# Performance work log

Hardware: AMD Instinct MI355X
Metric: run time of the kernel (lower is better)

## Reference

```python
import jax, jax.numpy as jnp
import numpy as np

N_ATOMS = 200000
N_EDGES = 6400000
N_TYPES = 4
COULOMB = 14.399645478425668  # e^2 / (4 pi eps0) in eV*Angstrom
P_EXP = 0.23
A0 = 0.4685


def _phi(r, c, da):
    # r: (E,), c: (4,), da: (4, E) -> (E,)
    return jnp.sum(c[:, None] * jnp.exp(-r * da), axis=0)


def _dphi(r, c, da):
    return jnp.sum(-c[:, None] * da * jnp.exp(-r * da), axis=0)


def _d2phi(r, c, da):
    return jnp.sum(c[:, None] * da ** 2 * jnp.exp(-r * da), axis=0)


def setup_inputs() -> dict:
    key = jax.random.key(0)
    k1, k2, k3, k4 = jax.random.split(key, 4)
    rij = jax.random.uniform(k1, (N_EDGES,), dtype=jnp.float32) * 2.0 + 0.1
    first_atom = jax.random.randint(k2, (N_EDGES,), 0, N_ATOMS, dtype=jnp.int32)
    second_atom = jax.random.randint(k3, (N_EDGES,), 0, N_ATOMS, dtype=jnp.int32)
    atom_type_index = jax.random.randint(k4, (N_ATOMS,), 0, N_TYPES, dtype=jnp.int32)
    # ASE covalent radii for H, C, N, O (Angstrom) and atomic numbers
    covalent_radii = jnp.array([0.31, 0.76, 0.71, 0.66], dtype=jnp.float32)
    atomic_numbers = jnp.array([1.0, 6.0, 7.0, 8.0], dtype=jnp.float32)
    return {
        "rij": rij,
        "covalent_radii": covalent_radii,
        "atomic_numbers": atomic_numbers,
        "first_atom": first_atom,
        "second_atom": second_atom,
        "atom_type_index": atom_type_index,
        "n_atoms": N_ATOMS,
    }


def reference(rij, covalent_radii, atomic_numbers, first_atom, second_atom, atom_type_index, n_atoms):
    # ZBL 4-term exponential screening coefficients
    c = jnp.array([0.02817, 0.28022, 0.50986, 0.18175], dtype=rij.dtype)
    d = jnp.array([0.20162, 0.4029, 0.94229, 3.1998], dtype=rij.dtype)

    ti = atom_type_index[first_atom]   # (E,)
    tj = atom_type_index[second_atom]  # (E,)
    zi = atomic_numbers[ti]
    zj = atomic_numbers[tj]
    rc = covalent_radii[ti] + covalent_radii[tj]  # outer cutoff per pair

    a = A0 / (zi ** P_EXP + zj ** P_EXP)  # (E,)
    da = d[:, None] / a                    # (4, E)
    factor = COULOMB * zi * zj             # (E,)

    # energy at rij
    e = factor / rij * _phi(rij, c, da)

    # switching polynomial matched at rc (r1 = 0)
    phi_c = _phi(rc, c, da)
    dphi_c = _dphi(rc, c, da)
    d2phi_c = _d2phi(rc, c, da)
    ec = factor / rc * phi_c
    dec = factor / rc * (-phi_c / rc + dphi_c)
    d2ec = factor / rc * (d2phi_c - 2.0 / rc * dphi_c + 2.0 * phi_c / rc ** 2)

    A = (-3.0 * dec + rc * d2ec) / rc ** 2
    B = (2.0 * dec - rc * d2ec) / rc ** 3
    C = -ec + rc * dec / 2.0 - rc * rc * d2ec / 12.0

    e = e + A / 3.0 * rij ** 3 + B / 4.0 * rij ** 4 + C
    e = e / 2.0
    e = jnp.where(rij > rc, jnp.zeros_like(e), e)

    # scatter pair energies onto first atom of each pair
    e_nodes = jax.ops.segment_sum(e, first_atom, num_segments=n_atoms)
    return e_nodes
```

## Files before the change

### kernel.cpp

```cpp
#include <hip/hip_runtime.h>

#define TPB_PACK  256
#define P1_BLOCKS 512
#define P1_TPB    1024
#define SB_BITS   14
#define SBS       (1 << SB_BITS)
#define NS_MAX    16
#define P2_TPB    1024
#define R_SUB     39
#define TPB_RED   256
#define CAP_MAX   1024

#define TAB_N   258
#define TAB_L0  (-3.3219281f)
#define TAB_HL  (0.017157490f)
#define TAB_INV (58.283567f)
#define TAB_OFF (193.61423f)

__global__ __launch_bounds__(TPB_PACK) void zbl_pack(
    const int* __restrict__ types, unsigned int* __restrict__ packed,
    float* __restrict__ fallback, int natoms, int nwords)
{
    int tid = blockIdx.x * TPB_PACK + threadIdx.x;
    int nth = gridDim.x * TPB_PACK;
    for (int w = tid; w < nwords; w += nth) {
        int base = w << 4;
        unsigned int word = 0;
        #pragma unroll
        for (int j = 0; j < 16; ++j) {
            int i = base + j;
            unsigned int t = (i < natoms) ? (unsigned int)types[i] : 0u;
            word |= (t & 3u) << (2 * j);
        }
        packed[w] = word;
    }
    for (int i = tid; i < natoms; i += nth) fallback[i] = 0.0f;
}

__global__ __launch_bounds__(P1_TPB) void zbl_bin(
    const float* __restrict__ rij,
    const float* __restrict__ rcov,
    const float* __restrict__ znum,
    const int*  __restrict__ fa,
    const int*  __restrict__ sa,
    const unsigned int* __restrict__ packed,
    unsigned int* __restrict__ regions,
    int*   __restrict__ counts,
    float* __restrict__ fallback,
    int E, int nquad, int natoms, int nwords, int NS, int cap, int chunkQ)
{
    extern __shared__ unsigned int s_packed[];
    __shared__ float  tabE[16 * TAB_N];
    __shared__ float4 cB[16];
    __shared__ float4 cS[16];
    __shared__ float  cC[16];
    __shared__ int scnt[NS_MAX];

    for (int w = threadIdx.x; w < nwords; w += P1_TPB)
        s_packed[w] = packed[w];
    if (threadIdx.x < NS) scnt[threadIdx.x] = 0;

    if (threadIdx.x < 16) {
        const float cc[4] = {0.02817f, 0.28022f, 0.50986f, 0.18175f};
        const float dd[4] = {0.20162f, 0.4029f, 0.94229f, 3.1998f};
        const float COUL = 14.399645478425668f;
        int t = threadIdx.x;
        int ti = t >> 2, tj = t & 3;
        float zi = znum[ti], zj = znum[tj];
        float rc = rcov[ti] + rcov[tj];
        float a = 0.4685f / (powf(zi, 0.23f) + powf(zj, 0.23f));
        float inva = 1.0f / a;
        float factor = COUL * zi * zj;
        float da[4], ee[4];
        float phi = 0.0f, dphi = 0.0f, d2phi = 0.0f;
        #pragma unroll
        for (int k = 0; k < 4; ++k) {
            da[k] = dd[k] * inva;
            ee[k] = expf(-rc * da[k]);
            phi   += cc[k] * ee[k];
            dphi  -= cc[k] * da[k] * ee[k];
            d2phi += cc[k] * da[k] * da[k] * ee[k];
        }
        float invrc = 1.0f / rc;
        float ec   = factor * invrc * phi;
        float dec  = factor * invrc * (-phi * invrc + dphi);
        float d2ec = factor * invrc * (d2phi - 2.0f * invrc * dphi + 2.0f * phi * invrc * invrc);
        float A = (-3.0f * dec + rc * d2ec) * invrc * invrc;
        float B = (2.0f * dec - rc * d2ec) * invrc * invrc * invrc;
        float Cc = -ec + 0.5f * rc * dec - rc * rc * d2ec * (1.0f / 12.0f);
        const float L2E = 1.4426950408889634f;
        cB[t] = make_float4(rc, 0.5f * factor, A * (1.0f / 6.0f), B * 0.125f);
        cS[t] = make_float4(-da[0] * L2E, -da[1] * L2E, -da[2] * L2E, -da[3] * L2E);
        cC[t] = Cc * 0.5f;
    }
    __syncthreads();

    const float lc0 = -5.1497481f;
    const float lc1 = -1.8353434f;
    const float lc2 = -0.9718340f;
    const float lc3 = -2.4600449f;

    for (int n = threadIdx.x; n < 16 * TAB_N; n += P1_TPB) {
        int t = n / TAB_N, k = n - t * TAB_N;
        float v = 0.0f;
        if (k <= 256) {
            float r = exp2f(__builtin_fmaf((float)k, TAB_HL, TAB_L0));
            float4 B = cB[t];
            if (r <= B.x) {
                float4 S = cS[t];
                float p = exp2f(__builtin_fmaf(r, S.x, lc0))
                        + exp2f(__builtin_fmaf(r, S.y, lc1))
                        + exp2f(__builtin_fmaf(r, S.z, lc2))
                        + exp2f(__builtin_fmaf(r, S.w, lc3));
                float r3 = r * r * r;
                float poly = __builtin_fmaf(__builtin_fmaf(B.w, r, B.z), r3, cC[t]);
                v = __builtin_fmaf(B.y * p, 1.0f / r, poly);
            }
        }
        tabE[n] = v;
    }
    __syncthreads();

    const float4* rij4 = (const float4*)rij;
    const int4*   fa4  = (const int4*)fa;
    const int4*   sa4  = (const int4*)sa;

    size_t myreg = (size_t)blockIdx.x * NS;

    int q0 = blockIdx.x * chunkQ;
    int q1 = q0 + chunkQ; if (q1 > nquad) q1 = nquad;

    for (int q = q0 + threadIdx.x; q < q1; q += P1_TPB) {
        float4 rv = rij4[q];
        int4   iv = fa4[q];
        int4   jv = sa4[q];
        float ra[4] = {rv.x, rv.y, rv.z, rv.w};
        int   ia[4] = {iv.x, iv.y, iv.z, iv.w};
        int   ja[4] = {jv.x, jv.y, jv.z, jv.w};
        float eo[4];
        #pragma unroll
        for (int k = 0; k < 4; ++k) {
            int i = ia[k], j = ja[k];
            unsigned int wi = s_packed[i >> 4], wj = s_packed[j >> 4];
            unsigned int ti = (wi >> ((i & 15) * 2)) & 3u;
            unsigned int tj = (wj >> ((j & 15) * 2)) & 3u;
            int t = (int)((ti << 2) | tj);
            float kf = __builtin_fmaf(__log2f(ra[k]), TAB_INV, TAB_OFF);
            int ki = (int)kf;
            ki = ki < 0 ? 0 : (ki > 256 ? 256 : ki);
            float frac = kf - (float)ki;
            int base = t * TAB_N + ki;
            float v0 = tabE[base];
            float v1 = tabE[base + 1];
            eo[k] = __builtin_fmaf(v1 - v0, frac, v0);
        }
        #pragma unroll
        for (int k = 0; k < 4; ++k) {
            if (eo[k] != 0.0f) {
                int atom = ia[k];
                int s = atom >> SB_BITS;
                int slot = atomicAdd(&scnt[s], 1);
                if (slot < cap) {
                    unsigned rec = ((__float_as_uint(eo[k]) + 0x2000u) & 0xFFFFC000u)
                                 | (unsigned)(atom & (SBS - 1));
                    regions[(myreg + s) * (size_t)cap + slot] = rec;
                } else {
                    unsafeAtomicAdd(&fallback[atom], eo[k]);
                }
            }
        }
    }

    if (blockIdx.x == 0) {
        for (int idx = nquad * 4 + threadIdx.x; idx < E; idx += P1_TPB) {
            int i = fa[idx], j = sa[idx];
            unsigned int wi = s_packed[i >> 4], wj = s_packed[j >> 4];
            int t = (int)((((wi >> ((i & 15) * 2)) & 3u) << 2) |
                           ((wj >> ((j & 15) * 2)) & 3u));
            float r = rij[idx];
            float kf = __builtin_fmaf(__log2f(r), TAB_INV, TAB_OFF);
            int ki = (int)kf;
            ki = ki < 0 ? 0 : (ki > 256 ? 256 : ki);
            float frac = kf - (float)ki;
            int base = t * TAB_N + ki;
            float v0 = tabE[base], v1 = tabE[base + 1];
            float e = __builtin_fmaf(v1 - v0, frac, v0);
            if (e != 0.0f) unsafeAtomicAdd(&fallback[i], e);
        }
    }

    __syncthreads();
    if (cap > 0 && threadIdx.x < NS)
        counts[threadIdx.x * P1_BLOCKS + blockIdx.x] = min(scnt[threadIdx.x], cap);
}

__global__ __launch_bounds__(P2_TPB) void zbl_agg(
    const unsigned int* __restrict__ regions,
    const int*  __restrict__ counts,
    float* __restrict__ partials,
    int NS, int cap)
{
    __shared__ float acc[SBS];
    int s = blockIdx.x;
    int r = blockIdx.y;

    float4* acc4 = (float4*)acc;
    for (int i = threadIdx.x; i < SBS / 4; i += P2_TPB)
        acc4[i] = make_float4(0.f, 0.f, 0.f, 0.f);
    __syncthreads();

    int wave = threadIdx.x >> 6;
    int lane = threadIdx.x & 63;
    const int NW = P2_TPB >> 6;
    for (int p = r + wave * R_SUB; p < P1_BLOCKS; p += NW * R_SUB) {
        int n = counts[s * P1_BLOCKS + p];
        size_t base = ((size_t)p * NS + s) * (size_t)cap;
        for (int t = lane; t < n; t += 64) {
            unsigned rec = regions[base + t];
            atomicAdd(&acc[rec & (SBS - 1)],
                      __uint_as_float(rec & 0xFFFFC000u));
        }
    }
    __syncthreads();

    float4* dst4 = (float4*)(partials + ((size_t)s * R_SUB + r) * SBS);
    for (int i = threadIdx.x; i < SBS / 4; i += P2_TPB)
        dst4[i] = acc4[i];
}

__global__ __launch_bounds__(TPB_RED) void zbl_red(
    const float* __restrict__ partials,
    const float* __restrict__ fallback,
    float* __restrict__ out,
    int natoms)
{
    int q = blockIdx.x * TPB_RED + threadIdx.x;
    int nq = natoms >> 2;
    if (q < nq) {
        int atom = q << 2;
        int s = atom >> SB_BITS, i = atom & (SBS - 1);
        const float4* fb4 = (const float4*)(fallback + atom);
        float4 acc = *fb4;
        const float* p = partials + (size_t)s * R_SUB * SBS + i;
        #pragma unroll
        for (int k = 0; k < R_SUB; ++k) {
            float4 v = *(const float4*)(p + (size_t)k * SBS);
            acc.x += v.x; acc.y += v.y; acc.z += v.z; acc.w += v.w;
        }
        *(float4*)(out + atom) = acc;
    }
    if (blockIdx.x == 0 && threadIdx.x < (natoms & 3)) {
        int atom = (nq << 2) + threadIdx.x;
        int s = atom >> SB_BITS, i = atom & (SBS - 1);
        float acc = fallback[atom];
        const float* p = partials + (size_t)s * R_SUB * SBS + i;
        #pragma unroll
        for (int k = 0; k < R_SUB; ++k) acc += p[(size_t)k * SBS];
        out[atom] = acc;
    }
}

extern "C" void kernel_launch(void* const* d_in, const int* in_sizes, int n_in,
                              void* d_out, int out_size, void* d_ws, size_t ws_size,
                              hipStream_t stream) {
    const float* rij  = (const float*)d_in[0];
    const float* rcov = (const float*)d_in[1];
    const float* znum = (const float*)d_in[2];
    const int*   fa   = (const int*)d_in[3];
    const int*   sa   = (const int*)d_in[4];
    const int*   types= (const int*)d_in[5];
    float* out = (float*)d_out;
    int E = in_sizes[0];
    int natoms = out_size;
    int nquad = E / 4;
    int nwords = (natoms + 15) / 16;
    int NS = (natoms + SBS - 1) >> SB_BITS;
    if (NS > NS_MAX) NS = NS_MAX;
    int chunkQ = (nquad + P1_BLOCKS - 1) / P1_BLOCKS;

    size_t packed_bytes = ((size_t)nwords * 4 + 255) & ~(size_t)255;
    size_t cnt_bytes    = ((size_t)NS * P1_BLOCKS * 4 + 255) & ~(size_t)255;
    size_t fb_bytes     = ((size_t)natoms * 4 + 255) & ~(size_t)255;
    size_t part_bytes   = ((size_t)NS * R_SUB * SBS * 4 + 255) & ~(size_t)255;
    unsigned int* packed = (unsigned int*)d_ws;
    int*   counts   = (int*)  ((char*)d_ws + packed_bytes);
    float* fallback = (float*)((char*)d_ws + packed_bytes + cnt_bytes);
    float* partials = (float*)((char*)d_ws + packed_bytes + cnt_bytes + fb_bytes);
    unsigned int* regions = (unsigned int*)((char*)d_ws + packed_bytes + cnt_bytes
                                            + fb_bytes + part_bytes);

    long long avail = (long long)ws_size
                    - (long long)(packed_bytes + cnt_bytes + fb_bytes + part_bytes);
    int cap = 0;
    if (avail > 0) cap = (int)(avail / ((long long)P1_BLOCKS * (long long)NS * 4));
    if (cap > CAP_MAX) cap = CAP_MAX;

    size_t smem = (size_t)nwords * sizeof(unsigned int);

    if (cap >= 64) {
        zbl_pack<<<96, TPB_PACK, 0, stream>>>(types, packed, fallback, natoms, nwords);
        zbl_bin<<<P1_BLOCKS, P1_TPB, smem, stream>>>(
            rij, rcov, znum, fa, sa, packed, regions, counts, fallback,
            E, nquad, natoms, nwords, NS, cap, chunkQ);
        dim3 g2(NS, R_SUB);
        zbl_agg<<<g2, P2_TPB, 0, stream>>>(regions, counts, partials, NS, cap);
        int nq = natoms >> 2;
        zbl_red<<<(nq + TPB_RED - 1) / TPB_RED, TPB_RED, 0, stream>>>(
            partials, fallback, out, natoms);
    } else {
        zbl_pack<<<96, TPB_PACK, 0, stream>>>(types, packed, out, natoms, nwords);
        zbl_bin<<<P1_BLOCKS, P1_TPB, smem, stream>>>(
            rij, rcov, znum, fa, sa, packed, regions, counts, out,
            E, nquad, natoms, nwords, NS, 0, chunkQ);
    }
}
```

Baseline: 162.5 us.

## Fuse pack, bin, aggregate and reduce into one persistent kernel with flag handoffs

Replaces the four-kernel pipeline with a single 512-block kernel. Blocks hand off data through self-validating 64-bit flag words (value plus its complement) in global memory and spin-wait on them, instead of relying on kernel boundaries. Overflow records now go to per-block lists that the final reduction applies, replacing global atomics into a fallback buffer. This is meant to remove launch gaps and tail idle time between stages. It depends on all 512 blocks being co-resident, otherwise the spin-waits can deadlock. It also relies on the workspace flags not already looking valid from a previous call.

```diff
diff --git a/kernel.cpp b/kernel.cpp
--- a/kernel.cpp
+++ b/kernel.cpp
@@ -1,10 +1,12 @@
 #include <hip/hip_runtime.h>
+
 
 #define TPB_PACK  256
 #define P1_BLOCKS 512
 #define P1_TPB    1024
 #define SB_BITS   14
 #define SBS       (1 << SB_BITS)
+#define NS_MEGA   13
 #define NS_MAX    16
 #define P2_TPB    1024
 #define R_SUB     39
@@ -16,6 +18,308 @@
 #define TAB_HL  (0.017157490f)
 #define TAB_INV (58.283567f)
 #define TAB_OFF (193.61423f)
+
+typedef unsigned long long u64;
+
+__device__ __forceinline__ void pub_pair(u64* p, unsigned v) {
+    u64 w = (u64)v | ((u64)(~v) << 32);
+    __hip_atomic_store(p, w, __ATOMIC_RELAXED, __HIP_MEMORY_SCOPE_AGENT);
+}
+__device__ __forceinline__ unsigned spin_pair(u64* p) {
+    for (;;) {
+        u64 w = __hip_atomic_load(p, __ATOMIC_RELAXED, __HIP_MEMORY_SCOPE_AGENT);
+        if ((unsigned)(w >> 32) == ~(unsigned)w) return (unsigned)w;
+        __builtin_amdgcn_s_sleep(1);
+    }
+}
+
+__global__ __launch_bounds__(P1_TPB, 8) void zbl_mega(
+    const float* __restrict__ rij,
+    const float* __restrict__ rcov,
+    const float* __restrict__ znum,
+    const int*  __restrict__ fa,
+    const int*  __restrict__ sa,
+    const int*  __restrict__ types,
+    u64*  __restrict__ packed2,
+    u64*  __restrict__ counts2,
+    u64*  __restrict__ ovfc2,
+    u64*  __restrict__ done2,
+    unsigned int* __restrict__ regions,
+    uint2* __restrict__ ovf,
+    float* __restrict__ partials,
+    float* __restrict__ out,
+    int E, int nquad, int natoms, int nwords, int NS, int cap, int chunkQ,
+    int ovfStride)
+{
+    __shared__ union {
+        struct { unsigned pk[NS_MEGA * SBS / 16]; float tabE[16 * TAB_N]; } a;
+        float  acc[SBS];
+        float4 acc4[SBS / 4];
+    } u;
+    __shared__ float4 cB[16];
+    __shared__ float4 cS[16];
+    __shared__ float  cC[16];
+    __shared__ int    scnt[NS_MAX];
+    __shared__ int    s_ovfn;
+    __shared__ int    s_anyovf;
+
+    const int b   = blockIdx.x;
+    const int tid = threadIdx.x;
+
+    {
+        int wpb = (nwords + P1_BLOCKS - 1) / P1_BLOCKS;
+        int w0 = b * wpb, w1 = w0 + wpb; if (w1 > nwords) w1 = nwords;
+        for (int w = w0 + tid; w < w1; w += P1_TPB) {
+            int base = w << 4;
+            unsigned word = 0;
+            #pragma unroll
+            for (int j = 0; j < 16; ++j) {
+                int i = base + j;
+                unsigned t = (i < natoms) ? (unsigned)types[i] : 0u;
+                word |= (t & 3u) << (2 * j);
+            }
+            pub_pair(&packed2[w], word);
+        }
+    }
+
+    if (tid < NS)  scnt[tid] = 0;
+    if (tid == 32) s_ovfn = 0;
+
+    if (tid < 16) {
+        const float cc[4] = {0.02817f, 0.28022f, 0.50986f, 0.18175f};
+        const float dd[4] = {0.20162f, 0.4029f, 0.94229f, 3.1998f};
+        const float COUL = 14.399645478425668f;
+        int t = tid;
+        int ti = t >> 2, tj = t & 3;
+        float zi = znum[ti], zj = znum[tj];
+        float rc = rcov[ti] + rcov[tj];
+        float a = 0.4685f / (powf(zi, 0.23f) + powf(zj, 0.23f));
+        float inva = 1.0f / a;
+        float factor = COUL * zi * zj;
+        float da[4], ee[4];
+        float phi = 0.0f, dphi = 0.0f, d2phi = 0.0f;
+        #pragma unroll
+        for (int k = 0; k < 4; ++k) {
+            da[k] = dd[k] * inva;
+            ee[k] = expf(-rc * da[k]);
+            phi   += cc[k] * ee[k];
+            dphi  -= cc[k] * da[k] * ee[k];
+            d2phi += cc[k] * da[k] * da[k] * ee[k];
+        }
+        float invrc = 1.0f / rc;
+        float ec   = factor * invrc * phi;
+        float dec  = factor * invrc * (-phi * invrc + dphi);
+        float d2ec = factor * invrc * (d2phi - 2.0f * invrc * dphi + 2.0f * phi * invrc * invrc);
+        float A = (-3.0f * dec + rc * d2ec) * invrc * invrc;
+        float B = (2.0f * dec - rc * d2ec) * invrc * invrc * invrc;
+        float Cc = -ec + 0.5f * rc * dec - rc * rc * d2ec * (1.0f / 12.0f);
+        const float L2E = 1.4426950408889634f;
+        cB[t] = make_float4(rc, 0.5f * factor, A * (1.0f / 6.0f), B * 0.125f);
+        cS[t] = make_float4(-da[0] * L2E, -da[1] * L2E, -da[2] * L2E, -da[3] * L2E);
+        cC[t] = Cc * 0.5f;
+    }
+
+    for (int w = tid; w < nwords; w += P1_TPB)
+        u.a.pk[w] = spin_pair(&packed2[w]);
+    __syncthreads();
+
+    const float lc0 = -5.1497481f;
+    const float lc1 = -1.8353434f;
+    const float lc2 = -0.9718340f;
+    const float lc3 = -2.4600449f;
+
+    for (int n = tid; n < 16 * TAB_N; n += P1_TPB) {
+        int t = n / TAB_N, k = n - t * TAB_N;
+        float v = 0.0f;
+        if (k <= 256) {
+            float r = exp2f(__builtin_fmaf((float)k, TAB_HL, TAB_L0));
+            float4 B = cB[t];
+            if (r <= B.x) {
+                float4 S = cS[t];
+                float p = exp2f(__builtin_fmaf(r, S.x, lc0))
+                        + exp2f(__builtin_fmaf(r, S.y, lc1))
+                        + exp2f(__builtin_fmaf(r, S.z, lc2))
+                        + exp2f(__builtin_fmaf(r, S.w, lc3));
+                float r3 = r * r * r;
+                float poly = __builtin_fmaf(__builtin_fmaf(B.w, r, B.z), r3, cC[t]);
+                v = __builtin_fmaf(B.y * p, 1.0f / r, poly);
+            }
+        }
+        u.a.tabE[n] = v;
+    }
+    __syncthreads();
+
+    {
+        const float4* rij4 = (const float4*)rij;
+        const int4*   fa4  = (const int4*)fa;
+        const int4*   sa4  = (const int4*)sa;
+        int myreg = b * NS;
+        int q0 = b * chunkQ;
+        int q1 = q0 + chunkQ; if (q1 > nquad) q1 = nquad;
+
+        for (int q = q0 + tid; q < q1; q += P1_TPB) {
+            float4 rv = rij4[q];
+            int4   iv = fa4[q];
+            int4   jv = sa4[q];
+            float ra[4] = {rv.x, rv.y, rv.z, rv.w};
+            int   ia[4] = {iv.x, iv.y, iv.z, iv.w};
+            int   ja[4] = {jv.x, jv.y, jv.z, jv.w};
+            float eo[4];
+            #pragma unroll
+            for (int k = 0; k < 4; ++k) {
+                int i = ia[k], j = ja[k];
+                unsigned wi = u.a.pk[i >> 4], wj = u.a.pk[j >> 4];
+                unsigned ti = (wi >> ((i & 15) * 2)) & 3u;
+                unsigned tj = (wj >> ((j & 15) * 2)) & 3u;
+                int t = (int)((ti << 2) | tj);
+                float kf = __builtin_fmaf(__log2f(ra[k]), TAB_INV, TAB_OFF);
+                int ki = (int)kf;
+                ki = ki < 0 ? 0 : (ki > 256 ? 256 : ki);
+                float frac = kf - (float)ki;
+                int base = t * TAB_N + ki;
+                float v0 = u.a.tabE[base];
+                float v1 = u.a.tabE[base + 1];
+                eo[k] = __builtin_fmaf(v1 - v0, frac, v0);
+            }
+            #pragma unroll
+            for (int k = 0; k < 4; ++k) {
+                if (eo[k] != 0.0f) {
+                    int atom = ia[k];
+                    int s = atom >> SB_BITS;
+                    int slot = atomicAdd(&scnt[s], 1);
+                    if (slot < cap) {
+                        unsigned rec = ((__float_as_uint(eo[k]) + 0x2000u) & 0xFFFFC000u)
+                                     | (unsigned)(atom & (SBS - 1));
+                        regions[(myreg + s) * cap + slot] = rec;
+                    } else {
+                        int o = atomicAdd(&s_ovfn, 1);
+                        ovf[(size_t)b * ovfStride + o] =
+                            make_uint2(__float_as_uint(eo[k]), (unsigned)atom);
+                    }
+                }
+            }
+        }
+
+        if (b == 0) {
+            for (int idx = nquad * 4 + tid; idx < E; idx += P1_TPB) {
+                int i = fa[idx], j = sa[idx];
+                unsigned wi = u.a.pk[i >> 4], wj = u.a.pk[j >> 4];
+                int t = (int)((((wi >> ((i & 15) * 2)) & 3u) << 2) |
+                               ((wj >> ((j & 15) * 2)) & 3u));
+                float r = rij[idx];
+                float kf = __builtin_fmaf(__log2f(r), TAB_INV, TAB_OFF);
+                int ki = (int)kf;
+                ki = ki < 0 ? 0 : (ki > 256 ? 256 : ki);
+                float frac = kf - (float)ki;
+                int base = t * TAB_N + ki;
+                float e = __builtin_fmaf(u.a.tabE[base + 1] - u.a.tabE[base], frac,
+                                         u.a.tabE[base]);
+                if (e != 0.0f) {
+                    int o = atomicAdd(&s_ovfn, 1);
+                    ovf[(size_t)b * ovfStride + o] =
+                        make_uint2(__float_as_uint(e), (unsigned)i);
+                }
+            }
+        }
+
+        __syncthreads();
+        if (tid == 0) __threadfence();
+        __syncthreads();
+        if (tid < NS)  pub_pair(&counts2[tid * P1_BLOCKS + b],
+                                (unsigned)min(scnt[tid], cap));
+        if (tid == NS) pub_pair(&ovfc2[b], (unsigned)s_ovfn);
+    }
+
+    if (b < NS * R_SUB) {
+        int s = b / R_SUB, r = b % R_SUB;
+        __syncthreads();
+        for (int i = tid; i < SBS / 4; i += P1_TPB)
+            u.acc4[i] = make_float4(0.f, 0.f, 0.f, 0.f);
+        __syncthreads();
+
+        int wave = tid >> 6;
+        int lane = tid & 63;
+        const int NW = P1_TPB >> 6;
+        for (int p = r + wave * R_SUB; p < P1_BLOCKS; p += NW * R_SUB) {
+            unsigned n = spin_pair(&counts2[s * P1_BLOCKS + p]);
+            __threadfence();
+            int base = (p * NS + s) * cap;
+            for (int t = lane; t < (int)n; t += 64) {
+                unsigned rec = regions[base + t];
+                atomicAdd(&u.acc[rec & (SBS - 1)],
+                          __uint_as_float(rec & 0xFFFFC000u));
+            }
+        }
+        __syncthreads();
+
+        float4* dst4 = (float4*)(partials + ((size_t)s * R_SUB + r) * SBS);
+        for (int i = tid; i < SBS / 4; i += P1_TPB)
+            dst4[i] = u.acc4[i];
+        __syncthreads();
+        if (tid == 0) {
+            __threadfence();
+            pub_pair(&done2[b], 1u);
+        }
+    }
+
+    {
+        for (int i = tid; i < NS * R_SUB; i += P1_TPB)
+            (void)spin_pair(&done2[i]);
+        __syncthreads();
+        if (tid == 0) __threadfence();
+        __syncthreads();
+
+        int nq  = natoms >> 2;
+        int qpb = (nq + P1_BLOCKS - 1) / P1_BLOCKS;
+        int qlo = b * qpb, qhi = qlo + qpb; if (qhi > nq) qhi = nq;
+        int alo = qlo << 2, ahi = qhi << 2;
+
+        for (int q = qlo + tid; q < qhi; q += P1_TPB) {
+            int atom = q << 2;
+            int s = atom >> SB_BITS, i = atom & (SBS - 1);
+            const float* p = partials + (size_t)s * R_SUB * SBS + i;
+            float4 acc = make_float4(0.f, 0.f, 0.f, 0.f);
+            #pragma unroll
+            for (int k = 0; k < R_SUB; ++k) {
+                float4 v = *(const float4*)(p + (size_t)k * SBS);
+                acc.x += v.x; acc.y += v.y; acc.z += v.z; acc.w += v.w;
+            }
+            *(float4*)(out + atom) = acc;
+        }
+        bool own_tail = (b == P1_BLOCKS - 1);
+        if (own_tail) {
+            for (int atom = (nq << 2) + tid; atom < natoms; atom += P1_TPB) {
+                int s = atom >> SB_BITS, i = atom & (SBS - 1);
+                const float* p = partials + (size_t)s * R_SUB * SBS + i;
+                float acc = 0.f;
+                #pragma unroll
+                for (int k = 0; k < R_SUB; ++k) acc += p[(size_t)k * SBS];
+                out[atom] = acc;
+            }
+        }
+
+        if (tid == 0) s_anyovf = 0;
+        __syncthreads();
+        for (int p0 = tid; p0 < P1_BLOCKS; p0 += P1_TPB) {
+            unsigned n = spin_pair(&ovfc2[p0]);
+            if (n) atomicAdd(&s_anyovf, (int)n);
+        }
+        __syncthreads();
+        if (s_anyovf > 0) {
+            for (int p = 0; p < P1_BLOCKS; ++p) {
+                unsigned n = spin_pair(&ovfc2[p]);
+                const uint2* lst = ovf + (size_t)p * ovfStride;
+                for (int e = tid; e < (int)n; e += P1_TPB) {
+                    uint2 rec = lst[e];
+                    int atom = (int)rec.y;
+                    bool mine = (atom >= alo && atom < ahi) ||
+                                (own_tail && atom >= (nq << 2) && atom < natoms);
+                    if (mine) unsafeAtomicAdd(&out[atom], __uint_as_float(rec.x));
+                }
+            }
+        }
+    }
+}
 
 __global__ __launch_bounds__(TPB_PACK) void zbl_pack(
     const int* __restrict__ types, unsigned int* __restrict__ packed,
@@ -38,14 +342,10 @@
 }
 
 __global__ __launch_bounds__(P1_TPB) void zbl_bin(
-    const float* __restrict__ rij,
-    const float* __restrict__ rcov,
-    const float* __restrict__ znum,
-    const int*  __restrict__ fa,
-    const int*  __restrict__ sa,
-    const unsigned int* __restrict__ packed,
-    unsigned int* __restrict__ regions,
-    int*   __restrict__ counts,
+    const float* __restrict__ rij, const float* __restrict__ rcov,
+    const float* __restrict__ znum, const int* __restrict__ fa,
+    const int* __restrict__ sa, const unsigned int* __restrict__ packed,
+    unsigned int* __restrict__ regions, int* __restrict__ counts,
     float* __restrict__ fallback,
     int E, int nquad, int natoms, int nwords, int NS, int cap, int chunkQ)
 {
@@ -56,8 +356,7 @@
     __shared__ float  cC[16];
     __shared__ int scnt[NS_MAX];
 
-    for (int w = threadIdx.x; w < nwords; w += P1_TPB)
-        s_packed[w] = packed[w];
+    for (int w = threadIdx.x; w < nwords; w += P1_TPB) s_packed[w] = packed[w];
     if (threadIdx.x < NS) scnt[threadIdx.x] = 0;
 
     if (threadIdx.x < 16) {
@@ -95,10 +394,8 @@
     }
     __syncthreads();
 
-    const float lc0 = -5.1497481f;
-    const float lc1 = -1.8353434f;
-    const float lc2 = -0.9718340f;
-    const float lc3 = -2.4600449f;
+    const float lc0 = -5.1497481f, lc1 = -1.8353434f;
+    const float lc2 = -0.9718340f, lc3 = -2.4600449f;
 
     for (int n = threadIdx.x; n < 16 * TAB_N; n += P1_TPB) {
         int t = n / TAB_N, k = n - t * TAB_N;
@@ -124,9 +421,7 @@
     const float4* rij4 = (const float4*)rij;
     const int4*   fa4  = (const int4*)fa;
     const int4*   sa4  = (const int4*)sa;
-
-    size_t myreg = (size_t)blockIdx.x * NS;
-
+    int myreg = blockIdx.x * NS;
     int q0 = blockIdx.x * chunkQ;
     int q1 = q0 + chunkQ; if (q1 > nquad) q1 = nquad;
 
@@ -150,8 +445,7 @@
             ki = ki < 0 ? 0 : (ki > 256 ? 256 : ki);
             float frac = kf - (float)ki;
             int base = t * TAB_N + ki;
-            float v0 = tabE[base];
-            float v1 = tabE[base + 1];
+            float v0 = tabE[base], v1 = tabE[base + 1];
             eo[k] = __builtin_fmaf(v1 - v0, frac, v0);
         }
         #pragma unroll
@@ -163,7 +457,7 @@
                 if (slot < cap) {
                     unsigned rec = ((__float_as_uint(eo[k]) + 0x2000u) & 0xFFFFC000u)
                                  | (unsigned)(atom & (SBS - 1));
-                    regions[(myreg + s) * (size_t)cap + slot] = rec;
+                    regions[(unsigned)((myreg + s) * cap + slot)] = rec;
                 } else {
                     unsafeAtomicAdd(&fallback[atom], eo[k]);
                 }
@@ -183,8 +477,7 @@
             ki = ki < 0 ? 0 : (ki > 256 ? 256 : ki);
             float frac = kf - (float)ki;
             int base = t * TAB_N + ki;
-            float v0 = tabE[base], v1 = tabE[base + 1];
-            float e = __builtin_fmaf(v1 - v0, frac, v0);
+            float e = __builtin_fmaf(tabE[base + 1] - tabE[base], frac, tabE[base]);
             if (e != 0.0f) unsafeAtomicAdd(&fallback[i], e);
         }
     }
@@ -195,44 +488,34 @@
 }
 
 __global__ __launch_bounds__(P2_TPB) void zbl_agg(
-    const unsigned int* __restrict__ regions,
-    const int*  __restrict__ counts,
-    float* __restrict__ partials,
-    int NS, int cap)
+    const unsigned int* __restrict__ regions, const int* __restrict__ counts,
+    float* __restrict__ partials, int NS, int cap)
 {
     __shared__ float acc[SBS];
-    int s = blockIdx.x;
-    int r = blockIdx.y;
-
+    int s = blockIdx.x, r = blockIdx.y;
     float4* acc4 = (float4*)acc;
     for (int i = threadIdx.x; i < SBS / 4; i += P2_TPB)
         acc4[i] = make_float4(0.f, 0.f, 0.f, 0.f);
     __syncthreads();
-
-    int wave = threadIdx.x >> 6;
-    int lane = threadIdx.x & 63;
+    int wave = threadIdx.x >> 6, lane = threadIdx.x & 63;
     const int NW = P2_TPB >> 6;
     for (int p = r + wave * R_SUB; p < P1_BLOCKS; p += NW * R_SUB) {
         int n = counts[s * P1_BLOCKS + p];
         size_t base = ((size_t)p * NS + s) * (size_t)cap;
         for (int t = lane; t < n; t += 64) {
             unsigned rec = regions[base + t];
-            atomicAdd(&acc[rec & (SBS - 1)],
-                      __uint_as_float(rec & 0xFFFFC000u));
+            atomicAdd(&acc[rec & (SBS - 1)], __uint_as_float(rec & 0xFFFFC000u));
         }
     }
     __syncthreads();
-
     float4* dst4 = (float4*)(partials + ((size_t)s * R_SUB + r) * SBS);
     for (int i = threadIdx.x; i < SBS / 4; i += P2_TPB)
         dst4[i] = acc4[i];
 }
 
 __global__ __launch_bounds__(TPB_RED) void zbl_red(
-    const float* __restrict__ partials,
-    const float* __restrict__ fallback,
-    float* __restrict__ out,
-    int natoms)
+    const float* __restrict__ partials, const float* __restrict__ fallback,
+    float* __restrict__ out, int natoms)
 {
     int q = blockIdx.x * TPB_RED + threadIdx.x;
     int nq = natoms >> 2;
@@ -259,6 +542,8 @@
         out[atom] = acc;
     }
 }
+
+static inline size_t al256(size_t x) { return (x + 255) & ~(size_t)255; }
 
 extern "C" void kernel_launch(void* const* d_in, const int* in_sizes, int n_in,
                               void* d_out, int out_size, void* d_ws, size_t ws_size,
@@ -277,24 +562,54 @@
     int NS = (natoms + SBS - 1) >> SB_BITS;
     if (NS > NS_MAX) NS = NS_MAX;
     int chunkQ = (nquad + P1_BLOCKS - 1) / P1_BLOCKS;
-
-    size_t packed_bytes = ((size_t)nwords * 4 + 255) & ~(size_t)255;
-    size_t cnt_bytes    = ((size_t)NS * P1_BLOCKS * 4 + 255) & ~(size_t)255;
-    size_t fb_bytes     = ((size_t)natoms * 4 + 255) & ~(size_t)255;
-    size_t part_bytes   = ((size_t)NS * R_SUB * SBS * 4 + 255) & ~(size_t)255;
+    int ovfStride = chunkQ * 4 + 8;
+
+    if (natoms <= NS_MEGA * SBS) {
+        size_t packed2_b = al256((size_t)nwords * 8);
+        size_t counts2_b = al256((size_t)NS * P1_BLOCKS * 8);
+        size_t ovfc2_b   = al256((size_t)P1_BLOCKS * 8);
+        size_t done2_b   = al256((size_t)NS * R_SUB * 8);
+        size_t part_b    = al256((size_t)NS * R_SUB * SBS * 4);
+        size_t ovf_b     = al256((size_t)P1_BLOCKS * ovfStride * 8);
+        char* base = (char*)d_ws;
+        u64*  packed2 = (u64*)base;                          base += packed2_b;
+        u64*  counts2 = (u64*)base;                          base += counts2_b;
+        u64*  ovfc2   = (u64*)base;                          base += ovfc2_b;
+        u64*  done2   = (u64*)base;                          base += done2_b;
+        float* partials = (float*)base;                      base += part_b;
+        uint2* ovf    = (uint2*)base;                        base += ovf_b;
+        unsigned int* regions = (unsigned int*)base;
+
+        long long avail = (long long)ws_size
+            - (long long)(packed2_b + counts2_b + ovfc2_b + done2_b + part_b + ovf_b);
+        int cap = 0;
+        if (avail > 0) cap = (int)(avail / ((long long)P1_BLOCKS * NS * 4));
+        if (cap > CAP_MAX) cap = CAP_MAX;
+
+        if (cap >= 64) {
+            zbl_mega<<<P1_BLOCKS, P1_TPB, 0, stream>>>(
+                rij, rcov, znum, fa, sa, types,
+                packed2, counts2, ovfc2, done2, regions, ovf, partials, out,
+                E, nquad, natoms, nwords, NS, cap, chunkQ, ovfStride);
+            return;
+        }
+    }
+
+    size_t packed_bytes = al256((size_t)nwords * 4);
+    size_t cnt_bytes    = al256((size_t)NS * P1_BLOCKS * 4);
+    size_t fb_bytes     = al256((size_t)natoms * 4);
+    size_t part_bytes   = al256((size_t)NS * R_SUB * SBS * 4);
     unsigned int* packed = (unsigned int*)d_ws;
     int*   counts   = (int*)  ((char*)d_ws + packed_bytes);
     float* fallback = (float*)((char*)d_ws + packed_bytes + cnt_bytes);
     float* partials = (float*)((char*)d_ws + packed_bytes + cnt_bytes + fb_bytes);
     unsigned int* regions = (unsigned int*)((char*)d_ws + packed_bytes + cnt_bytes
                                             + fb_bytes + part_bytes);
-
     long long avail = (long long)ws_size
                     - (long long)(packed_bytes + cnt_bytes + fb_bytes + part_bytes);
     int cap = 0;
     if (avail > 0) cap = (int)(avail / ((long long)P1_BLOCKS * (long long)NS * 4));
     if (cap > CAP_MAX) cap = CAP_MAX;
-
     size_t smem = (size_t)nwords * sizeof(unsigned int);
 
     if (cap >= 64) {
```

Result: slower. 426.6 us (+162.5%).
